# Kernel optimization log

Measured on AMD Instinct MI355X. Metric: run time of the kernel, lower is better.

The kernel has to match this reference:

```python
import jax, jax.numpy as jnp
import numpy as np

N_IN, N_HID, N_OUT = 2048, 4096, 1024
N_TOT = N_IN + N_HID + N_OUT
BATCH = 4096


def _structure_mask():
    # input -> {hidden, output}; hidden -> {hidden, output}; nothing feeds inputs,
    # outputs feed nothing.
    m = np.zeros((N_TOT, N_TOT), dtype=np.float32)
    m[0:N_IN, N_IN:N_TOT] = 1.0
    m[N_IN:N_IN + N_HID, N_IN:N_TOT] = 1.0
    return jnp.asarray(m)


def setup_inputs() -> dict:
    key = jax.random.key(0)
    kx, kw = jax.random.split(key)
    x = jax.random.normal(kx, (BATCH, N_IN), dtype=jnp.float32)
    weights = jax.random.normal(kw, (N_TOT, N_TOT), dtype=jnp.float32) * 0.1
    structure_mask = _structure_mask()
    return {"x": x, "weights": weights, "structure_mask": structure_mask}


def reference(x, weights, structure_mask):
    # Faithful to the torch forward: the per-neuron hidden loop reads the
    # activation vector BEFORE any hidden value is written, so every hidden
    # unit sees only [x, 0, 0]; outputs then see [x, hidden, 0].
    Wm = weights * structure_mask  # (N_TOT, N_TOT)
    B = x.shape[0]
    a0 = jnp.concatenate(
        [x, jnp.zeros((B, N_HID + N_OUT), dtype=x.dtype)], axis=1)  # (B, N_TOT)
    hidden = jax.nn.relu(a0 @ Wm[:, N_IN:N_IN + N_HID])             # (B, N_HID)
    a1 = jnp.concatenate(
        [x, hidden, jnp.zeros((B, N_OUT), dtype=x.dtype)], axis=1)  # (B, N_TOT)
    out = a1 @ Wm[:, N_IN + N_HID:]                                 # (B, N_OUT)
    return out
```

## Files before the change

kernel.cpp:

```cpp
#include <hip/hip_runtime.h>
#include <hip/hip_bf16.h>

#define N_IN  2048
#define N_HID 4096
#define N_OUT 1024
#define N_TOT 7168
#define BATCH 4096
#define LDA2  (N_IN + N_HID)

typedef __attribute__((ext_vector_type(8))) short short8;
typedef __attribute__((ext_vector_type(4))) float f32x4;

static __device__ __forceinline__ unsigned short f2bf(float f) {
  __hip_bfloat16 h = __float2bfloat16(f);
  return __builtin_bit_cast(unsigned short, h);
}

__global__ void conv_x_kernel(const float* __restrict__ x,
                              unsigned short* __restrict__ A2) {
  int idx = blockIdx.x * 256 + threadIdx.x;
  int row = idx >> 9;
  int col = (idx & 511) << 2;
  const float4 v = *(const float4*)(x + (size_t)row * N_IN + col);
  ushort4 o;
  o.x = f2bf(v.x); o.y = f2bf(v.y); o.z = f2bf(v.z); o.w = f2bf(v.w);
  *(ushort4*)(A2 + (size_t)row * LDA2 + col) = o;
}

__global__ void conv_t_kernel(const float* __restrict__ src, int lds_,
                              unsigned short* __restrict__ dst, int ldd,
                              int SK, int SN) {
  __shared__ float tile[32][33];
  const int t = threadIdx.x;
  const int k0 = blockIdx.y << 5, n0 = blockIdx.x << 5;
  const int r = t >> 3, c = (t & 7) << 2;
  const float4 v = *(const float4*)(src + (size_t)(k0 + r) * lds_ + n0 + c);
  tile[r][c] = v.x; tile[r][c + 1] = v.y; tile[r][c + 2] = v.z; tile[r][c + 3] = v.w;
  __syncthreads();
  ushort4 o;
  o.x = f2bf(tile[c][r]);
  o.y = f2bf(tile[c + 1][r]);
  o.z = f2bf(tile[c + 2][r]);
  o.w = f2bf(tile[c + 3][r]);
  *(ushort4*)(dst + (size_t)(n0 + r) * ldd + k0 + c) = o;
}

template <bool RELU_BF16>
__global__ __launch_bounds__(256)
void gemm_bt(const unsigned short* __restrict__ A, int lda,
             const unsigned short* __restrict__ Bt, int ldb,
             void* __restrict__ Cv, int ldc, int K) {
  __shared__ __align__(16) unsigned short As[128 * 64];
  __shared__ __align__(16) unsigned short Bs[128 * 64];

  const int tid  = threadIdx.x;
  const int lane = tid & 63;
  const int wave = tid >> 6;
  const int wy = wave >> 1, wx = wave & 1;
  const int lm = lane & 15, quad = lane >> 4;
  const int bm = blockIdx.y, bn = blockIdx.x;

  const int gi   = wave * 256 + lane;
  const int grow = gi >> 3;
  const int gcol = (gi & 7) << 3;

  const unsigned short* Ag = A  + (size_t)(bm * 128 + grow) * lda + gcol;
  const unsigned short* Bg = Bt + (size_t)(bn * 128 + grow) * ldb + gcol;
  unsigned short* Asl = As + wave * 2048;
  unsigned short* Bsl = Bs + wave * 2048;

  f32x4 acc[4][4];
#pragma unroll
  for (int i = 0; i < 4; ++i)
#pragma unroll
    for (int j = 0; j < 4; ++j)
      acc[i][j] = (f32x4){0.f, 0.f, 0.f, 0.f};

  for (int ko = 0; ko < K; ko += 64) {
    __syncthreads();
#pragma unroll
    for (int i = 0; i < 4; ++i) {
      __builtin_amdgcn_global_load_lds(
          (const __attribute__((address_space(1))) void*)(Ag + (size_t)(8 * i) * lda + ko),
          (__attribute__((address_space(3))) void*)(Asl + i * 512), 16, 0, 0);
      __builtin_amdgcn_global_load_lds(
          (const __attribute__((address_space(1))) void*)(Bg + (size_t)(8 * i) * ldb + ko),
          (__attribute__((address_space(3))) void*)(Bsl + i * 512), 16, 0, 0);
    }
    __syncthreads();

#pragma unroll
    for (int kk = 0; kk < 2; ++kk) {
      short8 av[4], bv[4];
#pragma unroll
      for (int mt = 0; mt < 4; ++mt)
        av[mt] = *(const short8*)(As + (wy * 64 + mt * 16 + lm) * 64 + kk * 32 + quad * 8);
#pragma unroll
      for (int nt = 0; nt < 4; ++nt)
        bv[nt] = *(const short8*)(Bs + (wx * 64 + nt * 16 + lm) * 64 + kk * 32 + quad * 8);
#pragma unroll
      for (int mt = 0; mt < 4; ++mt)
#pragma unroll
        for (int nt = 0; nt < 4; ++nt)
          acc[mt][nt] = __builtin_amdgcn_mfma_f32_16x16x32_bf16(
              av[mt], bv[nt], acc[mt][nt], 0, 0, 0);
    }
  }

  if (RELU_BF16) {
    unsigned short* C = (unsigned short*)Cv;
#pragma unroll
    for (int mt = 0; mt < 4; ++mt) {
      const int row0 = bm * 128 + wy * 64 + mt * 16 + quad * 4;
#pragma unroll
      for (int nt = 0; nt < 4; ++nt) {
        const int col = bn * 128 + wx * 64 + nt * 16 + lm;
#pragma unroll
        for (int r = 0; r < 4; ++r) {
          float v = acc[mt][nt][r];
          v = v > 0.f ? v : 0.f;
          C[(size_t)(row0 + r) * ldc + col] = f2bf(v);
        }
      }
    }
  } else {
    float* C = (float*)Cv;
#pragma unroll
    for (int mt = 0; mt < 4; ++mt) {
      const int row0 = bm * 128 + wy * 64 + mt * 16 + quad * 4;
#pragma unroll
      for (int nt = 0; nt < 4; ++nt) {
        const int col = bn * 128 + wx * 64 + nt * 16 + lm;
#pragma unroll
        for (int r = 0; r < 4; ++r)
          C[(size_t)(row0 + r) * ldc + col] = acc[mt][nt][r];
      }
    }
  }
}

extern "C" void kernel_launch(void* const* d_in, const int* in_sizes, int n_in,
                              void* d_out, int out_size, void* d_ws, size_t ws_size,
                              hipStream_t stream) {
  const float* x = (const float*)d_in[0];
  const float* W = (const float*)d_in[1];

  char* ws = (char*)d_ws;
  const size_t A2_BYTES  = (size_t)BATCH * LDA2 * 2;
  const size_t BT1_BYTES = (size_t)N_HID * N_IN * 2;
  unsigned short* A2  = (unsigned short*)ws;
  unsigned short* Bt1 = (unsigned short*)(ws + A2_BYTES);
  unsigned short* Bt2 = (unsigned short*)(ws + A2_BYTES + BT1_BYTES);

  conv_x_kernel<<<(BATCH * N_IN / 4) / 256, 256, 0, stream>>>(x, A2);

  conv_t_kernel<<<dim3(N_HID / 32, N_IN / 32), 256, 0, stream>>>(
      W + N_IN, N_TOT, Bt1, N_IN, N_IN, N_HID);

  conv_t_kernel<<<dim3(N_OUT / 32, LDA2 / 32), 256, 0, stream>>>(
      W + N_IN + N_HID, N_TOT, Bt2, LDA2, LDA2, N_OUT);

  gemm_bt<true><<<dim3(N_HID / 128, BATCH / 128), 256, 0, stream>>>(
      A2, LDA2, Bt1, N_IN, A2 + N_IN, LDA2, N_IN);

  gemm_bt<false><<<dim3(N_OUT / 128, BATCH / 128), 256, 0, stream>>>(
      A2, LDA2, Bt2, LDA2, d_out, N_OUT, LDA2);
}
```

Baseline: 573.8 us.

## Swizzle LDS tiles to avoid bank conflicts and split-K the output GEMM

Applies an XOR swizzle to the 16-byte chunk placement of A and B tiles in LDS, with matching swizzled reads, so MFMA fragment loads no longer conflict on the same banks. The second GEMM, which launched only 256 blocks, is split along K into two halves on gridDim.z and combined with float atomic adds into an output zeroed by a memset. This raises parallelism for the small GEMM at the cost of atomic traffic, an extra memset and nondeterministic summation order.

```diff
diff --git a/kernel.cpp b/kernel.cpp
--- a/kernel.cpp
+++ b/kernel.cpp
@@ -45,11 +45,11 @@
   *(ushort4*)(dst + (size_t)(n0 + r) * ldd + k0 + c) = o;
 }
 
-template <bool RELU_BF16>
+template <int WMODE>
 __global__ __launch_bounds__(256)
 void gemm_bt(const unsigned short* __restrict__ A, int lda,
              const unsigned short* __restrict__ Bt, int ldb,
-             void* __restrict__ Cv, int ldc, int K) {
+             void* __restrict__ Cv, int ldc, int Klen) {
   __shared__ __align__(16) unsigned short As[128 * 64];
   __shared__ __align__(16) unsigned short Bs[128 * 64];
 
@@ -59,13 +59,13 @@
   const int wy = wave >> 1, wx = wave & 1;
   const int lm = lane & 15, quad = lane >> 4;
   const int bm = blockIdx.y, bn = blockIdx.x;
+  const int ko0 = blockIdx.z * Klen;
 
-  const int gi   = wave * 256 + lane;
-  const int grow = gi >> 3;
-  const int gcol = (gi & 7) << 3;
+  const int grow = (wave << 5) + (lane >> 3);
+  const int gcol = ((lane & 7) ^ (lane >> 3)) << 3;
 
-  const unsigned short* Ag = A  + (size_t)(bm * 128 + grow) * lda + gcol;
-  const unsigned short* Bg = Bt + (size_t)(bn * 128 + grow) * ldb + gcol;
+  const unsigned short* Ag = A  + (size_t)(bm * 128 + grow) * lda + gcol + ko0;
+  const unsigned short* Bg = Bt + (size_t)(bn * 128 + grow) * ldb + gcol + ko0;
   unsigned short* Asl = As + wave * 2048;
   unsigned short* Bsl = Bs + wave * 2048;
 
@@ -76,7 +76,7 @@
     for (int j = 0; j < 4; ++j)
       acc[i][j] = (f32x4){0.f, 0.f, 0.f, 0.f};
 
-  for (int ko = 0; ko < K; ko += 64) {
+  for (int ko = 0; ko < Klen; ko += 64) {
     __syncthreads();
 #pragma unroll
     for (int i = 0; i < 4; ++i) {
@@ -93,11 +93,15 @@
     for (int kk = 0; kk < 2; ++kk) {
       short8 av[4], bv[4];
 #pragma unroll
-      for (int mt = 0; mt < 4; ++mt)
-        av[mt] = *(const short8*)(As + (wy * 64 + mt * 16 + lm) * 64 + kk * 32 + quad * 8);
+      for (int mt = 0; mt < 4; ++mt) {
+        const int r = wy * 64 + mt * 16 + lm;
+        av[mt] = *(const short8*)(As + r * 64 + (((kk * 4 + quad) ^ (lm & 7)) << 3));
+      }
 #pragma unroll
-      for (int nt = 0; nt < 4; ++nt)
-        bv[nt] = *(const short8*)(Bs + (wx * 64 + nt * 16 + lm) * 64 + kk * 32 + quad * 8);
+      for (int nt = 0; nt < 4; ++nt) {
+        const int r = wx * 64 + nt * 16 + lm;
+        bv[nt] = *(const short8*)(Bs + r * 64 + (((kk * 4 + quad) ^ (lm & 7)) << 3));
+      }
 #pragma unroll
       for (int mt = 0; mt < 4; ++mt)
 #pragma unroll
@@ -107,7 +111,7 @@
     }
   }
 
-  if (RELU_BF16) {
+  if (WMODE == 1) {
     unsigned short* C = (unsigned short*)Cv;
 #pragma unroll
     for (int mt = 0; mt < 4; ++mt) {
@@ -123,6 +127,19 @@
         }
       }
     }
+  } else if (WMODE == 0) {
+    float* C = (float*)Cv;
+#pragma unroll
+    for (int mt = 0; mt < 4; ++mt) {
+      const int row0 = bm * 128 + wy * 64 + mt * 16 + quad * 4;
+#pragma unroll
+      for (int nt = 0; nt < 4; ++nt) {
+        const int col = bn * 128 + wx * 64 + nt * 16 + lm;
+#pragma unroll
+        for (int r = 0; r < 4; ++r)
+          C[(size_t)(row0 + r) * ldc + col] = acc[mt][nt][r];
+      }
+    }
   } else {
     float* C = (float*)Cv;
 #pragma unroll
@@ -133,7 +150,7 @@
         const int col = bn * 128 + wx * 64 + nt * 16 + lm;
 #pragma unroll
         for (int r = 0; r < 4; ++r)
-          C[(size_t)(row0 + r) * ldc + col] = acc[mt][nt][r];
+          atomicAdd(&C[(size_t)(row0 + r) * ldc + col], acc[mt][nt][r]);
       }
     }
   }
@@ -152,6 +169,8 @@
   unsigned short* Bt1 = (unsigned short*)(ws + A2_BYTES);
   unsigned short* Bt2 = (unsigned short*)(ws + A2_BYTES + BT1_BYTES);
 
+  hipMemsetAsync(d_out, 0, (size_t)out_size * sizeof(float), stream);
+
   conv_x_kernel<<<(BATCH * N_IN / 4) / 256, 256, 0, stream>>>(x, A2);
 
   conv_t_kernel<<<dim3(N_HID / 32, N_IN / 32), 256, 0, stream>>>(
@@ -160,9 +179,9 @@
   conv_t_kernel<<<dim3(N_OUT / 32, LDA2 / 32), 256, 0, stream>>>(
       W + N_IN + N_HID, N_TOT, Bt2, LDA2, LDA2, N_OUT);
 
-  gemm_bt<true><<<dim3(N_HID / 128, BATCH / 128), 256, 0, stream>>>(
+  gemm_bt<1><<<dim3(N_HID / 128, BATCH / 128), 256, 0, stream>>>(
       A2, LDA2, Bt1, N_IN, A2 + N_IN, LDA2, N_IN);
 
-  gemm_bt<false><<<dim3(N_OUT / 128, BATCH / 128), 256, 0, stream>>>(
-      A2, LDA2, Bt2, LDA2, d_out, N_OUT, LDA2);
+  gemm_bt<2><<<dim3(N_OUT / 128, BATCH / 128, 2), 256, 0, stream>>>(
+      A2, LDA2, Bt2, LDA2, d_out, N_OUT, LDA2 / 2);
 }
```

New measurement: 518.0 us. -9.7%, faster.
